# Optimization experiments

Hardware: AMD Instinct MI355X
Metric: run time of the kernel (lower is better)

## Reference

```python
import jax, jax.numpy as jnp
import numpy as np
from jax import lax

RULE_START = 85
ALPHA = 0.2
SIGMA = 0.05


def setup_inputs() -> dict:
    key = jax.random.key(0)
    ks = jax.random.split(key, 10)
    T, B, H, NR, NO = 512, 256, 512, 20, 33
    D = RULE_START + NR
    s = lambda fan_in: 1.0 / np.sqrt(fan_in)
    return {
        "x": jax.random.normal(ks[0], (T, B, D), jnp.float32),
        "noise": jax.random.uniform(ks[1], (T, B, H), jnp.float32),
        "Ws_w": jax.random.normal(ks[2], (H, RULE_START), jnp.float32) * s(RULE_START),
        "Ws_b": jax.random.normal(ks[3], (H,), jnp.float32) * s(RULE_START),
        "Wr_w": jax.random.normal(ks[4], (H, NR), jnp.float32) * s(NR),
        "Wrec_w": jax.random.normal(ks[5], (H, H), jnp.float32) * s(H),
        "Wrec_b": jax.random.normal(ks[6], (H,), jnp.float32) * s(H),
        "mask": jnp.ones((H, H), jnp.float32),
        "Wout_w": jax.random.normal(ks[7], (NO, H), jnp.float32) * s(H),
        "Wout_b": jax.random.normal(ks[8], (NO,), jnp.float32) * s(H),
    }


def reference(x, noise, Ws_w, Ws_b, Wr_w, Wrec_w, Wrec_b, mask, Wout_w, Wout_b):
    # x: [T, B, rule_start + n_rule]
    sensory = x[:, :, :RULE_START]
    rule = x[:, :, RULE_START:]
    # input projections, batched over all T*B at once
    rnn_inputs = (jnp.einsum('tbd,hd->tbh', sensory, Ws_w) + Ws_b
                  + jnp.einsum('tbr,hr->tbh', rule, Wr_w))  # [T, B, H]
    masked_w = Wrec_w * mask  # [H, H]
    rec_noise = noise * SIGMA  # [T, B, H]

    h0 = jnp.zeros(rnn_inputs.shape[1:], rnn_inputs.dtype)  # [B, H]

    def step(h, inp):
        inp_t, noise_t = inp
        out = jax.nn.relu(inp_t + noise_t + h @ masked_w.T + Wrec_b)
        h_new = ALPHA * out + (1.0 - ALPHA) * h
        return h_new, h_new

    _, hidden_states = lax.scan(step, h0, (rnn_inputs, rec_noise))  # [T, B, H]
    out = jnp.einsum('tbh,oh->tbo', hidden_states, Wout_w) + Wout_b  # [T, B, n_output]
    return out
```

## Files before the change

kernel.cpp:

```cpp
#include <hip/hip_runtime.h>

#define TT 512
#define BB 256
#define HH 512
#define DD 105
#define RS 85
#define NRULE 20
#define NOUT 33
#define HALF 256

#define NFRAG_REC 512
#define NFRAG_IN  128
#define NFRAG_OUT 48
#define FRAG_IN_OFF  (NFRAG_REC)
#define FRAG_OUT_OFF (NFRAG_REC + NFRAG_IN)
#define NFRAG_TOT (NFRAG_REC + NFRAG_IN + NFRAG_OUT)

#define WP_BYTES    ((size_t)NFRAG_TOT * 1024)

#define PREC_OFF    WP_BYTES
#define PREC_STRIDE ((size_t)32768)
#define POUT_OFF    (PREC_OFF + 32 * PREC_STRIDE)
#define POUT_STRIDE ((size_t)9216)
#define EXCH_BYTES  (32 * PREC_STRIDE + 16 * POUT_STRIDE)

#define BPRE_OFF    WP_BYTES
#define BPRE_BYTES  ((size_t)TT * 16 * 16 * 512 * 2)
#define SNEED       (BPRE_OFF + BPRE_BYTES)

#define RETRY_GUARD 100000

typedef __bf16 bf16x8 __attribute__((ext_vector_type(8)));
typedef float  f32x4  __attribute__((ext_vector_type(4)));
typedef unsigned long long u64;
typedef unsigned short us;

__device__ __forceinline__ us f2bf(float f) {
  unsigned u = __builtin_bit_cast(unsigned, f);
  u += 0x7FFFu + ((u >> 16) & 1u);
  return (us)(u >> 16);
}
__device__ __forceinline__ float bf2f(us v) {
  return __builtin_bit_cast(float, (unsigned)v << 16);
}
__device__ __forceinline__ u64 ld_agent(const u64* p) {
  return __hip_atomic_load(p, __ATOMIC_RELAXED, __HIP_MEMORY_SCOPE_AGENT);
}
__device__ __forceinline__ void st_agent(u64* p, u64 v) {
  __hip_atomic_store(p, v, __ATOMIC_RELAXED, __HIP_MEMORY_SCOPE_AGENT);
}
__device__ __forceinline__ float bfhi(unsigned w) {
  return __builtin_bit_cast(float, w & 0xffff0000u);
}
__device__ __forceinline__ unsigned pkv(float v, unsigned tag) {
  return ((unsigned)f2bf(v) << 16) | tag;
}
__device__ __forceinline__ int tags4_ok(u64 v0, u64 v1, u64 v2, u64 v3, unsigned tag) {
  return (((unsigned)v0 & 0xffffu) == tag) & (((unsigned)(v0 >> 32) & 0xffffu) == tag)
       & (((unsigned)v1 & 0xffffu) == tag) & (((unsigned)(v1 >> 32) & 0xffffu) == tag)
       & (((unsigned)v2 & 0xffffu) == tag) & (((unsigned)(v2 >> 32) & 0xffffu) == tag)
       & (((unsigned)v3 & 0xffffu) == tag) & (((unsigned)(v3 >> 32) & 0xffffu) == tag);
}
__device__ __forceinline__ int tags2_ok(u64 v0, u64 v1, unsigned tag) {
  return (((unsigned)v0 & 0xffffu) == tag) & (((unsigned)(v0 >> 32) & 0xffffu) == tag)
       & (((unsigned)v1 & 0xffffu) == tag) & (((unsigned)(v1 >> 32) & 0xffffu) == tag);
}

__global__ void pack_weights(const float* __restrict__ Ws_w, const float* __restrict__ Wr_w,
                             const float* __restrict__ Wrec_w, const float* __restrict__ mask,
                             const float* __restrict__ Wout_w, us* __restrict__ wp)
{
  int gid = blockIdx.x * blockDim.x + threadIdx.x;
  if (gid >= NFRAG_TOT * 64) return;
  int f = gid >> 6, lane = gid & 63;
  int m16 = lane & 15, kg = lane >> 4;
  float v[8];
  if (f < NFRAG_REC) {
    int mt = f >> 4, kt = f & 15;
    int m = mt * 16 + m16, k0 = kt * 32 + kg * 8;
#pragma unroll
    for (int j = 0; j < 8; ++j) {
      int k = k0 + j;
      v[j] = Wrec_w[m * HH + k] * mask[m * HH + k];
    }
  } else if (f < FRAG_OUT_OFF) {
    int ff = f - FRAG_IN_OFF;
    int mt = ff >> 2, kt = ff & 3;
    int m = mt * 16 + m16, k0 = kt * 32 + kg * 8;
#pragma unroll
    for (int j = 0; j < 8; ++j) {
      int k = k0 + j;
      float val = 0.f;
      if (k < RS) val = Ws_w[m * RS + k];
      else if (k < DD) val = Wr_w[m * NRULE + (k - RS)];
      v[j] = val;
    }
  } else {
    int ff = f - FRAG_OUT_OFF;
    int mt = ff >> 4, kt = ff & 15;
    int m = mt * 16 + m16, k0 = kt * 32 + kg * 8;
#pragma unroll
    for (int j = 0; j < 8; ++j) {
      int k = k0 + j;
      v[j] = (m < NOUT) ? Wout_w[m * HH + k] : 0.f;
    }
  }
  unsigned o[4];
#pragma unroll
  for (int j = 0; j < 4; ++j)
    o[j] = (unsigned)f2bf(v[2 * j]) | ((unsigned)f2bf(v[2 * j + 1]) << 16);
  uint4 st = make_uint4(o[0], o[1], o[2], o[3]);
  *reinterpret_cast<uint4*>(wp + (size_t)f * 512 + lane * 8) = st;
}

__global__ __launch_bounds__(512)
void precompute_pre(const float* __restrict__ x, const float* __restrict__ noise,
                    const float* __restrict__ Ws_b, const float* __restrict__ Wrec_b,
                    const us* __restrict__ wp, us* __restrict__ pre)
{
  __shared__ alignas(16) us x_lds[16 * 128];
  const int t  = blockIdx.x >> 4;
  const int gg = blockIdx.x & 15;
  const int gb = gg * 16;
  const int tid = threadIdx.x;
  const int wv = tid >> 6, lane = tid & 63;
  const int bcol = lane & 15, krow = lane >> 4;
  const int sw = (bcol & 7) << 3;
  const uint4* wp4 = reinterpret_cast<const uint4*>(wp);

  for (int i = tid; i < 16 * 128; i += 512) x_lds[i] = 0;
  __syncthreads();
  if (tid < 420) {
    f32x4 xv = reinterpret_cast<const f32x4*>(x + ((size_t)t * BB + gb) * DD)[tid];
#pragma unroll
    for (int j = 0; j < 4; ++j) {
      int e = tid * 4 + j;
      int b = e / DD, k = e - b * DD;
      x_lds[b * 128 + (k ^ ((b & 7) << 3))] = f2bf(xv[j]);
    }
  }
  __syncthreads();

  us ov[16];
#pragma unroll
  for (int jj = 0; jj < 4; ++jj) {
    int m = wv * 4 + jj;
    f32x4 acc = {0.f, 0.f, 0.f, 0.f};
#pragma unroll
    for (int kx = 0; kx < 4; ++kx) {
      int k0 = kx * 32 + krow * 8;
      bf16x8 xb = __builtin_bit_cast(bf16x8,
          *reinterpret_cast<const uint4*>(&x_lds[bcol * 128 + (k0 ^ sw)]));
      bf16x8 aw = __builtin_bit_cast(bf16x8, wp4[(FRAG_IN_OFF + m * 4 + kx) * 64 + lane]);
      acc = __builtin_amdgcn_mfma_f32_16x16x32_bf16(aw, xb, acc, 0, 0, 0);
    }
    int h0 = m * 16 + krow * 4;
    f32x4 b1 = *reinterpret_cast<const f32x4*>(Ws_b + h0);
    f32x4 b2 = *reinterpret_cast<const f32x4*>(Wrec_b + h0);
    f32x4 nz = *reinterpret_cast<const f32x4*>(noise + ((size_t)t * BB + gb + bcol) * HH + h0);
#pragma unroll
    for (int r = 0; r < 4; ++r)
      ov[jj * 4 + r] = f2bf(acc[r] + b1[r] + b2[r] + 0.05f * nz[r]);
  }
  us* dst = pre + (((size_t)t * 16 + gg) * 512 + tid) * 16;
  *reinterpret_cast<uint4*>(dst)     = *reinterpret_cast<uint4*>(&ov[0]);
  *reinterpret_cast<uint4*>(dst + 8) = *reinterpret_cast<uint4*>(&ov[8]);
}

__global__ __launch_bounds__(512, 2)
void rnn_seq16(unsigned char* __restrict__ ws)
{
  __shared__ alignas(16) us h_lds[16 * 512];
  __shared__ alignas(16) us wlds[128 * 512];

  const int tid  = threadIdx.x;
  const int wv   = tid >> 6;
  const int lane = tid & 63;
  const int bcol = lane & 15;
  const int krow = lane >> 4;
  const int g    = blockIdx.x;
  const int sw   = (bcol & 7) << 3;
  const uint4* wp4 = reinterpret_cast<const uint4*>(ws);
  us* pre = (us*)(ws + BPRE_OFF);

  for (int i = tid; i < 16 * 512; i += 512) h_lds[i] = 0;
  for (int c = tid; c < 128 * 64; c += 512) {
    int fl = c >> 6, l = c & 63;
    int w = fl >> 4, kt = fl & 15;
    int mt = 4 * w + 3;
    uint4 v = wp4[(mt * 16 + kt) * 64 + l];
    *reinterpret_cast<uint4*>(&wlds[fl * 512 + l * 8]) = v;
  }

  bf16x8 wreg[3][16];
#pragma unroll
  for (int j = 0; j < 3; ++j)
#pragma unroll
    for (int kt = 0; kt < 16; ++kt)
      wreg[j][kt] = __builtin_bit_cast(bf16x8, wp4[((4 * wv + j) * 16 + kt) * 64 + lane]);

  int h0[4];
#pragma unroll
  for (int j = 0; j < 4; ++j) h0[j] = (4 * wv + j) * 16 + krow * 4;

  __syncthreads();

  const size_t tstride = (size_t)16 * 512 * 16;
  us* pio = pre + ((size_t)g * 512 + tid) * 16;

  uint4 pA[2];
  pA[0] = *reinterpret_cast<const uint4*>(pio);
  pA[1] = *reinterpret_cast<const uint4*>(pio + 8);

  uint4 hs[2] = {};

#pragma unroll 1
  for (int t = 0; t < TT; ++t) {
    if (t > 0) {
      us* hout = pio + (size_t)(t - 1) * tstride;
      *reinterpret_cast<uint4*>(hout)     = hs[0];
      *reinterpret_cast<uint4*>(hout + 8) = hs[1];
    }
    uint4 pB[2];
    if (t + 1 < TT) {
      const us* pn = pio + (size_t)(t + 1) * tstride;
      pB[0] = *reinterpret_cast<const uint4*>(pn);
      pB[1] = *reinterpret_cast<const uint4*>(pn + 8);
    }

    f32x4 acc[4];
#pragma unroll
    for (int j = 0; j < 4; ++j) acc[j] = f32x4{0.f, 0.f, 0.f, 0.f};
#pragma unroll
    for (int kt = 0; kt < 16; ++kt) {
      bf16x8 hb = __builtin_bit_cast(bf16x8,
          *reinterpret_cast<const uint4*>(&h_lds[bcol * 512 + ((kt * 32 + krow * 8) ^ sw)]));
      acc[0] = __builtin_amdgcn_mfma_f32_16x16x32_bf16(wreg[0][kt], hb, acc[0], 0, 0, 0);
      acc[1] = __builtin_amdgcn_mfma_f32_16x16x32_bf16(wreg[1][kt], hb, acc[1], 0, 0, 0);
      acc[2] = __builtin_amdgcn_mfma_f32_16x16x32_bf16(wreg[2][kt], hb, acc[2], 0, 0, 0);
      bf16x8 wl = __builtin_bit_cast(bf16x8,
          *reinterpret_cast<const uint4*>(&wlds[(wv * 16 + kt) * 512 + lane * 8]));
      acc[3] = __builtin_amdgcn_mfma_f32_16x16x32_bf16(wl, hb, acc[3], 0, 0, 0);
    }

    {
      const us* pa = reinterpret_cast<const us*>(pA);
      us* hh = reinterpret_cast<us*>(hs);
#pragma unroll
      for (int j = 0; j < 4; ++j)
#pragma unroll
        for (int r = 0; r < 4; ++r) {
          int s = j * 4 + r;
          float v = acc[j][r] + bf2f(pa[s]);
          v = fmaxf(v, 0.f);
          hh[s] = f2bf(0.2f * v + 0.8f * bf2f(hh[s]));
        }
    }
    __syncthreads();
    {
      const us* hh = reinterpret_cast<const us*>(hs);
#pragma unroll
      for (int j = 0; j < 4; ++j) {
        *reinterpret_cast<ushort4*>(&h_lds[bcol * 512 + (h0[j] ^ sw)]) =
            make_ushort4(hh[j * 4], hh[j * 4 + 1], hh[j * 4 + 2], hh[j * 4 + 3]);
      }
    }
    pA[0] = pB[0];
    pA[1] = pB[1];
    __syncthreads();
  }

  {
    us* hout = pio + (size_t)(TT - 1) * tstride;
    *reinterpret_cast<uint4*>(hout)     = hs[0];
    *reinterpret_cast<uint4*>(hout + 8) = hs[1];
  }
}

__global__ __launch_bounds__(256)
void out_gemm(const us* __restrict__ hid, const us* __restrict__ wp,
              const float* __restrict__ Wout_b, float* __restrict__ out)
{
  __shared__ alignas(16) us t_lds[16 * 512];
  const int tid = threadIdx.x;
  const int wv = tid >> 6, lane = tid & 63;
  const int bcol = lane & 15, krow = lane >> 4;
  const int tg = blockIdx.x;
  const int t = tg >> 4, g = tg & 15;
  const int sw = (bcol & 7) << 3;
  const uint4* wp4 = reinterpret_cast<const uint4*>(wp);

#pragma unroll
  for (int q = 0; q < 2; ++q) {
    int cc = tid + q * 256;
    const us* src = hid + (size_t)tg * 8192 + (size_t)cc * 16;
    uint4 v0 = *reinterpret_cast<const uint4*>(src);
    uint4 v1 = *reinterpret_cast<const uint4*>(src + 8);
    us vs[16];
    *reinterpret_cast<uint4*>(&vs[0]) = v0;
    *reinterpret_cast<uint4*>(&vs[8]) = v1;
    int b = cc & 15, kr = (cc >> 4) & 3;
    int swb = (b & 7) << 3;
#pragma unroll
    for (int jj = 0; jj < 4; ++jj) {
      int m = (cc >> 6) * 4 + jj;
      int h = m * 16 + kr * 4;
      *reinterpret_cast<ushort4*>(&t_lds[b * 512 + (h ^ swb)]) =
          make_ushort4(vs[jj * 4], vs[jj * 4 + 1], vs[jj * 4 + 2], vs[jj * 4 + 3]);
    }
  }
  __syncthreads();
  if (wv < 3) {
    f32x4 po = {0.f, 0.f, 0.f, 0.f};
#pragma unroll
    for (int kt = 0; kt < 16; ++kt) {
      bf16x8 hb = __builtin_bit_cast(bf16x8,
          *reinterpret_cast<const uint4*>(&t_lds[bcol * 512 + ((kt * 32 + krow * 8) ^ sw)]));
      bf16x8 ao = __builtin_bit_cast(bf16x8, wp4[(FRAG_OUT_OFF + wv * 16 + kt) * 64 + lane]);
      po = __builtin_amdgcn_mfma_f32_16x16x32_bf16(ao, hb, po, 0, 0, 0);
    }
#pragma unroll
    for (int r = 0; r < 4; ++r) {
      int o = wv * 16 + krow * 4 + r;
      if (o < NOUT)
        out[((size_t)t * BB + g * 16 + bcol) * NOUT + o] = po[r] + Wout_b[o];
    }
  }
}

__global__ __launch_bounds__(512, 2)
void rnn_fused(const float* __restrict__ x, const float* __restrict__ noise,
               const float* __restrict__ Ws_b, const float* __restrict__ Wrec_b,
               const float* __restrict__ Wout_b, unsigned char* __restrict__ ws,
               float* __restrict__ out)
{
  __shared__ alignas(16) us h_lds[16 * HALF];
  __shared__ alignas(16) us x_lds[2][16 * 128];
  __shared__ alignas(16) us win_lds[64 * 512];
  __shared__ alignas(16) us wout_lds[24 * 512];

  const int tid  = threadIdx.x;
  const int wv   = tid >> 6;
  const int lane = tid & 63;
  const int bcol = lane & 15;
  const int krow = lane >> 4;
  const int bid  = blockIdx.x;
  const int g    = bid & 15;
  const int hf   = bid >> 4;
  const int gb   = g * 16;
  const int hbase = hf * HALF;
  const int sw   = (bcol & 7) << 3;
  const bool outduty = (hf == 0);

  const uint4* wp4 = reinterpret_cast<const uint4*>(ws);
  u64* prec_own = (u64*)(ws + PREC_OFF + (size_t)bid * PREC_STRIDE);
  const u64* prec_par = (const u64*)(ws + PREC_OFF + (size_t)(bid ^ 16) * PREC_STRIDE);
  u64* pout_buf = (u64*)(ws + POUT_OFF + (size_t)g * POUT_STRIDE);

  for (int i = tid; i < 16 * HALF; i += 512) h_lds[i] = 0;
  {
    us* xz = &x_lds[0][0];
    for (int i = tid; i < 2 * 16 * 128; i += 512) xz[i] = 0;
  }
  for (int c = tid; c < 64 * 64; c += 512) {
    int fl = c >> 6, l = c & 63;
    uint4 w = wp4[(FRAG_IN_OFF + hf * 64 + fl) * 64 + l];
    *reinterpret_cast<uint4*>(&win_lds[fl * 512 + l * 8]) = w;
  }
  for (int c = tid; c < 24 * 64; c += 512) {
    int fl = c >> 6, l = c & 63;
    int mt_o = fl >> 3, kto = fl & 7;
    uint4 w = wp4[(FRAG_OUT_OFF + mt_o * 16 + hf * 8 + kto) * 64 + l];
    *reinterpret_cast<uint4*>(&wout_lds[fl * 512 + l * 8]) = w;
  }

  bf16x8 wreg_own[2][8], wreg_par[2][8];
#pragma unroll
  for (int j = 0; j < 2; ++j)
#pragma unroll
    for (int kt = 0; kt < 8; ++kt) {
      wreg_own[j][kt] = __builtin_bit_cast(bf16x8,
          wp4[((hf * 16 + 2 * wv + j) * 16 + (hf * 8 + kt)) * 64 + lane]);
      wreg_par[j][kt] = __builtin_bit_cast(bf16x8,
          wp4[(((1 - hf) * 16 + 2 * wv + j) * 16 + (hf * 8 + kt)) * 64 + lane]);
    }

  float bias_reg[2][4];
#pragma unroll
  for (int j = 0; j < 2; ++j)
#pragma unroll
    for (int r = 0; r < 4; ++r) {
      int h = hbase + (2 * wv + j) * 16 + krow * 4 + r;
      bias_reg[j][r] = Ws_b[h] + Wrec_b[h];
    }
  float woutb[4];
#pragma unroll
  for (int r = 0; r < 4; ++r) {
    int o = wv * 16 + krow * 4 + r;
    woutb[r] = (outduty && wv < 3 && o < NOUT) ? Wout_b[o] : 0.f;
  }

  const int rbase = bcol * 256 + 2 * wv * 16 + krow * 4;
  const int ri = rbase >> 1;
  const int oi = (bcol * 48 + wv * 16 + krow * 4) >> 1;

  float hreg[2][4] = {};
  f32x4 nrA[2], nrB[2];
  f32x4 po_hold = {0.f, 0.f, 0.f, 0.f};

  __syncthreads();

  if (tid < 420) {
    f32x4 xv = reinterpret_cast<const f32x4*>(x + (size_t)gb * DD)[tid];
#pragma unroll
    for (int j = 0; j < 4; ++j) {
      int e = tid * 4 + j;
      int b = e / DD, k = e - b * DD;
      x_lds[0][b * 128 + (k ^ ((b & 7) << 3))] = f2bf(xv[j]);
    }
  }
  {
    const float* nb = noise + ((size_t)gb + bcol) * HH + hbase + krow * 4;
#pragma unroll
    for (int j = 0; j < 2; ++j)
      nrA[j] = *reinterpret_cast<const f32x4*>(nb + (2 * wv + j) * 16);
  }
  __syncthreads();

#pragma unroll 1
  for (int t = 0; t < TT; ++t) {
    const int cur = t & 1;
    const unsigned tag = (unsigned)t;
    u64* prec_slot = prec_own + (size_t)(t & 1) * 2048;
    const u64* precp_slot = prec_par + (size_t)(t & 1) * 2048;
    f32x4 xs = {0.f, 0.f, 0.f, 0.f};
    if (t + 1 < TT) {
      if (tid < 420)
        xs = reinterpret_cast<const f32x4*>(x + ((size_t)(t + 1) * BB + gb) * DD)[tid];
      const float* nb = noise + (((size_t)(t + 1)) * BB + gb + bcol) * HH + hbase + krow * 4;
#pragma unroll
      for (int j = 0; j < 2; ++j)
        nrB[j] = *reinterpret_cast<const f32x4*>(nb + (2 * wv + j) * 16);
    }

    if (t > 0) {
      f32x4 pc0 = {0.f,0.f,0.f,0.f}, pc1 = {0.f,0.f,0.f,0.f};
#pragma unroll
      for (int kto = 0; kto < 8; ++kto) {
        int k0 = kto * 32 + krow * 8;
        bf16x8 hb = __builtin_bit_cast(bf16x8,
            *reinterpret_cast<const uint4*>(&h_lds[bcol * HALF + (k0 ^ sw)]));
        pc0 = __builtin_amdgcn_mfma_f32_16x16x32_bf16(wreg_par[0][kto], hb, pc0, 0, 0, 0);
        pc1 = __builtin_amdgcn_mfma_f32_16x16x32_bf16(wreg_par[1][kto], hb, pc1, 0, 0, 0);
      }
      st_agent(prec_slot + ri,     (u64)pkv(pc0[0], tag) | ((u64)pkv(pc0[1], tag) << 32));
      st_agent(prec_slot + ri + 1, (u64)pkv(pc0[2], tag) | ((u64)pkv(pc0[3], tag) << 32));
      st_agent(prec_slot + ri + 8, (u64)pkv(pc1[0], tag) | ((u64)pkv(pc1[1], tag) << 32));
      st_agent(prec_slot + ri + 9, (u64)pkv(pc1[2], tag) | ((u64)pkv(pc1[3], tag) << 32));
    }

    f32x4 acc[2];
    acc[0] = f32x4{0.f,0.f,0.f,0.f};
    acc[1] = f32x4{0.f,0.f,0.f,0.f};
#pragma unroll
    for (int kto = 0; kto < 8; ++kto) {
      int k0 = kto * 32 + krow * 8;
      bf16x8 hb = __builtin_bit_cast(bf16x8,
          *reinterpret_cast<const uint4*>(&h_lds[bcol * HALF + (k0 ^ sw)]));
      acc[0] = __builtin_amdgcn_mfma_f32_16x16x32_bf16(wreg_own[0][kto], hb, acc[0], 0, 0, 0);
      acc[1] = __builtin_amdgcn_mfma_f32_16x16x32_bf16(wreg_own[1][kto], hb, acc[1], 0, 0, 0);
    }
#pragma unroll
    for (int kx = 0; kx < 4; ++kx) {
      int k0 = kx * 32 + krow * 8;
      bf16x8 xb = __builtin_bit_cast(bf16x8,
          *reinterpret_cast<const uint4*>(&x_lds[cur][bcol * 128 + (k0 ^ sw)]));
#pragma unroll
      for (int j = 0; j < 2; ++j) {
        bf16x8 aw = __builtin_bit_cast(bf16x8,
            *reinterpret_cast<const uint4*>(&win_lds[((2 * wv + j) * 4 + kx) * 512 + lane * 8]));
        acc[j] = __builtin_amdgcn_mfma_f32_16x16x32_bf16(aw, xb, acc[j], 0, 0, 0);
      }
    }

    f32x4 po = {0.f, 0.f, 0.f, 0.f};
    if (t > 0 && wv < 3) {
#pragma unroll
      for (int kto = 0; kto < 8; ++kto) {
        int k0 = kto * 32 + krow * 8;
        bf16x8 hb = __builtin_bit_cast(bf16x8,
            *reinterpret_cast<const uint4*>(&h_lds[bcol * HALF + (k0 ^ sw)]));
        bf16x8 ao = __builtin_bit_cast(bf16x8,
            *reinterpret_cast<const uint4*>(&wout_lds[(wv * 8 + kto) * 512 + lane * 8]));
        po = __builtin_amdgcn_mfma_f32_16x16x32_bf16(ao, hb, po, 0, 0, 0);
      }
    }

    f32x4 pa0 = {0.f,0.f,0.f,0.f}, pa1 = {0.f,0.f,0.f,0.f};
    if (t > 0) {
      u64 v0, v1, v2, v3;
      int guard = RETRY_GUARD;
      for (;;) {
        v0 = ld_agent(precp_slot + ri);
        v1 = ld_agent(precp_slot + ri + 1);
        v2 = ld_agent(precp_slot + ri + 8);
        v3 = ld_agent(precp_slot + ri + 9);
        if (__all(tags4_ok(v0, v1, v2, v3, tag)) || --guard == 0) break;
        __builtin_amdgcn_s_sleep(1);
      }
      pa0[0] = bfhi((unsigned)v0); pa0[1] = bfhi((unsigned)(v0 >> 32));
      pa0[2] = bfhi((unsigned)v1); pa0[3] = bfhi((unsigned)(v1 >> 32));
      pa1[0] = bfhi((unsigned)v2); pa1[1] = bfhi((unsigned)(v2 >> 32));
      pa1[2] = bfhi((unsigned)v3); pa1[3] = bfhi((unsigned)(v3 >> 32));
      if (!outduty && wv < 3) {
        u64* ps = pout_buf + (size_t)(t & 1) * 384;
        st_agent(ps + oi,     (u64)pkv(po[0], tag) | ((u64)pkv(po[1], tag) << 32));
        st_agent(ps + oi + 1, (u64)pkv(po[2], tag) | ((u64)pkv(po[3], tag) << 32));
      }
    }

    __syncthreads();

#pragma unroll
    for (int j = 0; j < 2; ++j) {
      us hsv[4];
      f32x4 pa = j ? pa1 : pa0;
#pragma unroll
      for (int r = 0; r < 4; ++r) {
        float v = acc[j][r] + pa[r] + bias_reg[j][r] + 0.05f * nrA[j][r];
        v = fmaxf(v, 0.f);
        float hn = 0.2f * v + 0.8f * hreg[j][r];
        hreg[j][r] = hn;
        hsv[r] = f2bf(hn);
      }
      int hloc = (2 * wv + j) * 16 + krow * 4;
      *reinterpret_cast<ushort4*>(&h_lds[bcol * HALF + (hloc ^ sw)]) =
          make_ushort4(hsv[0], hsv[1], hsv[2], hsv[3]);
    }
    if (t + 1 < TT && tid < 420) {
#pragma unroll
      for (int j = 0; j < 4; ++j) {
        int e = tid * 4 + j;
        int b = e / DD, k = e - b * DD;
        x_lds[cur ^ 1][b * 128 + (k ^ ((b & 7) << 3))] = f2bf(xs[j]);
      }
    }
#pragma unroll
    for (int j = 0; j < 2; ++j) nrA[j] = nrB[j];

    if (outduty && wv < 3 && t >= 2) {
      const unsigned otag = (unsigned)(t - 1);
      const u64* ps = pout_buf + (size_t)((t - 1) & 1) * 384;
      u64 w0, w1;
      int guard = RETRY_GUARD;
      for (;;) {
        w0 = ld_agent(ps + oi);
        w1 = ld_agent(ps + oi + 1);
        if (__all(tags2_ok(w0, w1, otag)) || --guard == 0) break;
        __builtin_amdgcn_s_sleep(1);
      }
      float pr[4] = { bfhi((unsigned)w0), bfhi((unsigned)(w0 >> 32)),
                      bfhi((unsigned)w1), bfhi((unsigned)(w1 >> 32)) };
#pragma unroll
      for (int r = 0; r < 4; ++r) {
        int o = wv * 16 + krow * 4 + r;
        if (o < NOUT)
          out[((size_t)(t - 2) * BB + gb + bcol) * NOUT + o] = po_hold[r] + pr[r] + woutb[r];
      }
    }
    if (outduty && wv < 3 && t > 0) po_hold = po;

    __syncthreads();
  }

  if (!outduty && wv < 3) {
    f32x4 po = {0.f, 0.f, 0.f, 0.f};
#pragma unroll
    for (int kto = 0; kto < 8; ++kto) {
      int k0 = kto * 32 + krow * 8;
      bf16x8 hb = __builtin_bit_cast(bf16x8,
          *reinterpret_cast<const uint4*>(&h_lds[bcol * HALF + (k0 ^ sw)]));
      bf16x8 ao = __builtin_bit_cast(bf16x8,
          *reinterpret_cast<const uint4*>(&wout_lds[(wv * 8 + kto) * 512 + lane * 8]));
      po = __builtin_amdgcn_mfma_f32_16x16x32_bf16(ao, hb, po, 0, 0, 0);
    }
    const unsigned tagT = (unsigned)TT;
    u64* ps = pout_buf + (size_t)2 * 384;
    st_agent(ps + oi,     (u64)pkv(po[0], tagT) | ((u64)pkv(po[1], tagT) << 32));
    st_agent(ps + oi + 1, (u64)pkv(po[2], tagT) | ((u64)pkv(po[3], tagT) << 32));
  }
  if (outduty && wv < 3) {
    {
      const unsigned otag = (unsigned)(TT - 1);
      const u64* ps = pout_buf + (size_t)((TT - 1) & 1) * 384;
      u64 w0, w1;
      int guard = RETRY_GUARD;
      for (;;) {
        w0 = ld_agent(ps + oi);
        w1 = ld_agent(ps + oi + 1);
        if (__all(tags2_ok(w0, w1, otag)) || --guard == 0) break;
        __builtin_amdgcn_s_sleep(1);
      }
      float pr[4] = { bfhi((unsigned)w0), bfhi((unsigned)(w0 >> 32)),
                      bfhi((unsigned)w1), bfhi((unsigned)(w1 >> 32)) };
#pragma unroll
      for (int r = 0; r < 4; ++r) {
        int o = wv * 16 + krow * 4 + r;
        if (o < NOUT)
          out[((size_t)(TT - 2) * BB + gb + bcol) * NOUT + o] = po_hold[r] + pr[r] + woutb[r];
      }
    }
    {
      f32x4 po = {0.f, 0.f, 0.f, 0.f};
#pragma unroll
      for (int kto = 0; kto < 8; ++kto) {
        int k0 = kto * 32 + krow * 8;
        bf16x8 hb = __builtin_bit_cast(bf16x8,
            *reinterpret_cast<const uint4*>(&h_lds[bcol * HALF + (k0 ^ sw)]));
        bf16x8 ao = __builtin_bit_cast(bf16x8,
            *reinterpret_cast<const uint4*>(&wout_lds[(wv * 8 + kto) * 512 + lane * 8]));
        po = __builtin_amdgcn_mfma_f32_16x16x32_bf16(ao, hb, po, 0, 0, 0);
      }
      const unsigned tagT = (unsigned)TT;
      const u64* ps = pout_buf + (size_t)2 * 384;
      u64 w0, w1;
      int guard = RETRY_GUARD;
      for (;;) {
        w0 = ld_agent(ps + oi);
        w1 = ld_agent(ps + oi + 1);
        if (__all(tags2_ok(w0, w1, tagT)) || --guard == 0) break;
        __builtin_amdgcn_s_sleep(1);
      }
      float pr[4] = { bfhi((unsigned)w0), bfhi((unsigned)(w0 >> 32)),
                      bfhi((unsigned)w1), bfhi((unsigned)(w1 >> 32)) };
#pragma unroll
      for (int r = 0; r < 4; ++r) {
        int o = wv * 16 + krow * 4 + r;
        if (o < NOUT)
          out[((size_t)(TT - 1) * BB + gb + bcol) * NOUT + o] = po[r] + pr[r] + woutb[r];
      }
    }
  }
}

extern "C" void kernel_launch(void* const* d_in, const int* in_sizes, int n_in,
                              void* d_out, int out_size, void* d_ws, size_t ws_size,
                              hipStream_t stream) {
  (void)in_sizes; (void)n_in; (void)out_size;
  const float* x      = (const float*)d_in[0];
  const float* noise  = (const float*)d_in[1];
  const float* Ws_w   = (const float*)d_in[2];
  const float* Ws_b   = (const float*)d_in[3];
  const float* Wr_w   = (const float*)d_in[4];
  const float* Wrec_w = (const float*)d_in[5];
  const float* Wrec_b = (const float*)d_in[6];
  const float* mask   = (const float*)d_in[7];
  const float* Wout_w = (const float*)d_in[8];
  const float* Wout_b = (const float*)d_in[9];
  unsigned char* ws   = (unsigned char*)d_ws;
  float* out          = (float*)d_out;

  pack_weights<<<(NFRAG_TOT * 64 + 255) / 256, 256, 0, stream>>>(
      Ws_w, Wr_w, Wrec_w, mask, Wout_w, (us*)ws);

  if (ws_size >= (size_t)SNEED) {
    us* pre = (us*)(ws + BPRE_OFF);
    precompute_pre<<<TT * 16, 512, 0, stream>>>(x, noise, Ws_b, Wrec_b, (us*)ws, pre);
    rnn_seq16<<<16, 512, 0, stream>>>(ws);
    out_gemm<<<TT * 16, 256, 0, stream>>>(pre, (us*)ws, Wout_b, out);
  } else {
    hipMemsetAsync(ws + PREC_OFF, 0, EXCH_BYTES, stream);
    rnn_fused<<<32, 512, 0, stream>>>(x, noise, Ws_b, Wrec_b, Wout_b, ws, out);
  }
}
```

Before: 1.708 ms.

## Double-buffer hidden state in LDS to drop one barrier per recurrent step

Ping-pongs the hidden-state LDS buffer so each timestep reads one copy and writes the other. This removes one of the two __syncthreads per step. To make room in LDS, two K-tiles of the fourth weight column block move into registers and the LDS weight cache shrinks from 128 to 112 fragments. It also raises wave priority around the MFMA loop and loads the precomputed input for the current step instead of prefetching the next one, which may expose load latency and adds register pressure.

```diff
diff --git a/kernel.cpp b/kernel.cpp
--- a/kernel.cpp
+++ b/kernel.cpp
@@ -170,8 +170,8 @@
 __global__ __launch_bounds__(512, 2)
 void rnn_seq16(unsigned char* __restrict__ ws)
 {
-  __shared__ alignas(16) us h_lds[16 * 512];
-  __shared__ alignas(16) us wlds[128 * 512];
+  __shared__ alignas(16) us h_lds[2][16 * 512];
+  __shared__ alignas(16) us wlds[112 * 512];
 
   const int tid  = threadIdx.x;
   const int wv   = tid >> 6;
@@ -183,10 +183,13 @@
   const uint4* wp4 = reinterpret_cast<const uint4*>(ws);
   us* pre = (us*)(ws + BPRE_OFF);
 
-  for (int i = tid; i < 16 * 512; i += 512) h_lds[i] = 0;
-  for (int c = tid; c < 128 * 64; c += 512) {
+  {
+    us* hz = &h_lds[0][0];
+    for (int i = tid; i < 2 * 16 * 512; i += 512) hz[i] = 0;
+  }
+  for (int c = tid; c < 112 * 64; c += 512) {
     int fl = c >> 6, l = c & 63;
-    int w = fl >> 4, kt = fl & 15;
+    int w = fl / 14, kt = fl % 14;
     int mt = 4 * w + 3;
     uint4 v = wp4[(mt * 16 + kt) * 64 + l];
     *reinterpret_cast<uint4*>(&wlds[fl * 512 + l * 8]) = v;
@@ -198,6 +201,10 @@
 #pragma unroll
     for (int kt = 0; kt < 16; ++kt)
       wreg[j][kt] = __builtin_bit_cast(bf16x8, wp4[((4 * wv + j) * 16 + kt) * 64 + lane]);
+  bf16x8 wx[2];
+#pragma unroll
+  for (int j = 0; j < 2; ++j)
+    wx[j] = __builtin_bit_cast(bf16x8, wp4[((4 * wv + 3) * 16 + 14 + j) * 64 + lane]);
 
   int h0[4];
 #pragma unroll
@@ -208,40 +215,43 @@
   const size_t tstride = (size_t)16 * 512 * 16;
   us* pio = pre + ((size_t)g * 512 + tid) * 16;
 
-  uint4 pA[2];
-  pA[0] = *reinterpret_cast<const uint4*>(pio);
-  pA[1] = *reinterpret_cast<const uint4*>(pio + 8);
-
   uint4 hs[2] = {};
 
 #pragma unroll 1
   for (int t = 0; t < TT; ++t) {
+    const int cur = t & 1;
     if (t > 0) {
       us* hout = pio + (size_t)(t - 1) * tstride;
       *reinterpret_cast<uint4*>(hout)     = hs[0];
       *reinterpret_cast<uint4*>(hout + 8) = hs[1];
     }
-    uint4 pB[2];
-    if (t + 1 < TT) {
-      const us* pn = pio + (size_t)(t + 1) * tstride;
-      pB[0] = *reinterpret_cast<const uint4*>(pn);
-      pB[1] = *reinterpret_cast<const uint4*>(pn + 8);
+    uint4 pA[2];
+    {
+      const us* pn = pio + (size_t)t * tstride;
+      pA[0] = *reinterpret_cast<const uint4*>(pn);
+      pA[1] = *reinterpret_cast<const uint4*>(pn + 8);
     }
 
     f32x4 acc[4];
 #pragma unroll
     for (int j = 0; j < 4; ++j) acc[j] = f32x4{0.f, 0.f, 0.f, 0.f};
+    __builtin_amdgcn_s_setprio(1);
 #pragma unroll
     for (int kt = 0; kt < 16; ++kt) {
       bf16x8 hb = __builtin_bit_cast(bf16x8,
-          *reinterpret_cast<const uint4*>(&h_lds[bcol * 512 + ((kt * 32 + krow * 8) ^ sw)]));
+          *reinterpret_cast<const uint4*>(&h_lds[cur][bcol * 512 + ((kt * 32 + krow * 8) ^ sw)]));
       acc[0] = __builtin_amdgcn_mfma_f32_16x16x32_bf16(wreg[0][kt], hb, acc[0], 0, 0, 0);
       acc[1] = __builtin_amdgcn_mfma_f32_16x16x32_bf16(wreg[1][kt], hb, acc[1], 0, 0, 0);
       acc[2] = __builtin_amdgcn_mfma_f32_16x16x32_bf16(wreg[2][kt], hb, acc[2], 0, 0, 0);
-      bf16x8 wl = __builtin_bit_cast(bf16x8,
-          *reinterpret_cast<const uint4*>(&wlds[(wv * 16 + kt) * 512 + lane * 8]));
+      bf16x8 wl;
+      if (kt < 14)
+        wl = __builtin_bit_cast(bf16x8,
+            *reinterpret_cast<const uint4*>(&wlds[(wv * 14 + kt) * 512 + lane * 8]));
+      else
+        wl = wx[kt - 14];
       acc[3] = __builtin_amdgcn_mfma_f32_16x16x32_bf16(wl, hb, acc[3], 0, 0, 0);
     }
+    __builtin_amdgcn_s_setprio(0);
 
     {
       const us* pa = reinterpret_cast<const us*>(pA);
@@ -256,17 +266,14 @@
           hh[s] = f2bf(0.2f * v + 0.8f * bf2f(hh[s]));
         }
     }
-    __syncthreads();
     {
       const us* hh = reinterpret_cast<const us*>(hs);
 #pragma unroll
       for (int j = 0; j < 4; ++j) {
-        *reinterpret_cast<ushort4*>(&h_lds[bcol * 512 + (h0[j] ^ sw)]) =
+        *reinterpret_cast<ushort4*>(&h_lds[cur ^ 1][bcol * 512 + (h0[j] ^ sw)]) =
             make_ushort4(hh[j * 4], hh[j * 4 + 1], hh[j * 4 + 2], hh[j * 4 + 3]);
       }
     }
-    pA[0] = pB[0];
-    pA[1] = pB[1];
     __syncthreads();
   }
 
```

Result: no change. 1.704 ms (-0.2%).
